# Performance work log

Hardware: AMD Instinct MI355X
Metric: run time of the kernel (lower is better)

## Reference

```python
import jax, jax.numpy as jnp
import numpy as np

B, C_IN, C_OUT, N, E = 4, 16, 16, 16384, 131072
EDGE_CH = 2 * (C_IN + 2)  # 36


def setup_inputs() -> dict:
    key = jax.random.key(0)
    ks = jax.random.split(key, 7)
    u = jax.random.normal(ks[0], (B, C_IN, N), dtype=jnp.float32)
    grid = jax.random.uniform(ks[1], (B, N, 2), dtype=jnp.float32)
    edge_index = jax.random.randint(ks[2], (2, E), 0, N, dtype=jnp.int32)
    k_w1 = jax.random.normal(ks[3], (EDGE_CH, 8), dtype=jnp.float32) / np.sqrt(EDGE_CH)
    k_b1 = jnp.zeros((8,), dtype=jnp.float32)
    k_w2 = jax.random.normal(ks[4], (8, C_IN * C_OUT), dtype=jnp.float32) / np.sqrt(8.0)
    k_b2 = jnp.zeros((C_IN * C_OUT,), dtype=jnp.float32)
    root_w = jax.random.normal(ks[5], (C_IN, C_OUT), dtype=jnp.float32) / np.sqrt(C_IN)
    return {"u": u, "grid": grid, "edge_index": edge_index,
            "k_w1": k_w1, "k_b1": k_b1, "k_w2": k_w2, "k_b2": k_b2,
            "root_w": root_w}


def reference(u, grid, edge_index, k_w1, k_b1, k_w2, k_b2, root_w):
    b, c_in, n = u.shape
    c_out = root_w.shape[1]
    # [B, C, N] -> [B*N, C]
    x = jnp.transpose(u, (0, 2, 1)).reshape(b * n, c_in)
    pf = jnp.concatenate([x, grid.reshape(-1, 2)], axis=-1)  # [B*N, C+2]
    # faithful to edge_index_one.repeat(1,1,B).view(2,-1): tile, NO batch offset
    ei = jnp.tile(edge_index, (1, b))  # [2, E*B]
    src, dst = ei[0], ei[1]
    attr = jnp.concatenate([pf[src], pf[dst]], axis=-1)  # [EB, 2*(C+2)]
    h = jax.nn.gelu(attr @ k_w1 + k_b1, approximate=False)
    w = (h @ k_w2 + k_b2).reshape(-1, c_in, c_out)  # [EB, C_in, C_out]
    msg = jnp.einsum('ec,eco->eo', x[src], w)  # per-edge matmul
    # scatter-mean onto targets (PyG aggr='mean'; empty -> 0)
    num_seg = b * n
    agg = jax.ops.segment_sum(msg, dst, num_segments=num_seg)
    cnt = jax.ops.segment_sum(jnp.ones((msg.shape[0],), msg.dtype), dst,
                              num_segments=num_seg)
    agg = agg / jnp.maximum(cnt, 1.0)[:, None]
    out = agg + x @ root_w  # root_weight=True, bias=False
    return jnp.transpose(out.reshape(b, n, c_out), (0, 2, 1))
```

## Files before the change

### kernel.cpp

```cpp
#include <hip/hip_runtime.h>
#include <math.h>

#define NN 16384
#define NE 131072
#define STRIDE 40

typedef unsigned int uint32;
typedef unsigned short ushort;

__device__ __forceinline__ ushort f2bf(float f) {
    uint32 b = __float_as_uint(f);
    b += 0x7FFFu + ((b >> 16) & 1u);
    return (ushort)(b >> 16);
}
__device__ __forceinline__ float bf2f(ushort u) {
    return __uint_as_float(((uint32)u) << 16);
}


__global__ __launch_bounds__(256) void d1_pre(
        const float* __restrict__ u, const float* __restrict__ grid,
        const float* __restrict__ kw1, const float* __restrict__ kb1,
        const float* __restrict__ kw2, const float* __restrict__ kb2,
        const float* __restrict__ root_w,
        float* __restrict__ H, float* __restrict__ Bterm,
        ushort* __restrict__ Gh, int* __restrict__ cursor,
        float* __restrict__ out) {
    int bid = blockIdx.x;
    int t = threadIdx.x;

    if (bid < 256) {
        __shared__ float s_pf[64 * 18];
        __shared__ float s_w1[288];
        __shared__ float s_b1[8];
        __shared__ float s_w2t[16 * 132];
        __shared__ float s_b2t[256];
        int n0 = bid * 64;

        if (t < 64) cursor[n0 + t] = 0;

        for (int i = t; i < 1024; i += 256) {
            int c = i >> 6, nl = i & 63;
            s_pf[nl * 18 + c] = u[c * NN + n0 + nl];
        }
        if (t < 128) {
            int nl = t >> 1, g = t & 1;
            s_pf[nl * 18 + 16 + g] = grid[2 * (n0 + nl) + g];
        }
        if (t < 8) s_b1[t] = kb1[t];
        {
            s_w1[t] = kw1[t];
            if (t < 32) s_w1[256 + t] = kw1[256 + t];
        }
        for (int i = t; i < 2048; i += 256) {
            int j = i >> 8, rem = i & 255, ci = rem >> 4, co = rem & 15;
            s_w2t[co * 132 + j * 16 + ci] = kw2[i];
        }
        {
            int ci = t >> 4, co = t & 15;
            s_b2t[co * 16 + ci] = kb2[ci * 16 + co];
        }
        __syncthreads();

        int co = t & 15;
        #pragma unroll
        for (int s = 0; s < 4; ++s) {
            int nl = s * 16 + (t >> 4);
            int n = n0 + nl;
            const float* pfl = s_pf + nl * 18;
            float x[16];
            #pragma unroll
            for (int ci = 0; ci < 16; ++ci) x[ci] = pfl[ci];

            {
                float bt = 0.0f;
                const float4* bv = (const float4*)(s_b2t + co * 16);
                #pragma unroll
                for (int q = 0; q < 4; ++q) {
                    float4 w = bv[q];
                    bt += x[4*q] * w.x + x[4*q+1] * w.y + x[4*q+2] * w.z + x[4*q+3] * w.w;
                }
                Bterm[n * 16 + co] = bt;
            }
            #pragma unroll
            for (int j = 0; j < 8; ++j) {
                float g = 0.0f;
                const float4* wv = (const float4*)(s_w2t + co * 132 + j * 16);
                #pragma unroll
                for (int q = 0; q < 4; ++q) {
                    float4 w = wv[q];
                    g += x[4*q] * w.x + x[4*q+1] * w.y + x[4*q+2] * w.z + x[4*q+3] * w.w;
                }
                Gh[(size_t)n * 128 + j * 16 + co] = f2bf(g);
            }
            if (co < 8) {
                float hv = s_b1[co];
                #pragma unroll
                for (int i = 0; i < 18; ++i) hv += pfl[i] * s_w1[i * 8 + co];
                H[n * 16 + co] = hv;
            } else {
                int jj = co - 8;
                float hv = 0.0f;
                #pragma unroll
                for (int i = 0; i < 18; ++i) hv += pfl[i] * s_w1[(18 + i) * 8 + jj];
                H[n * 16 + co] = hv;
            }
        }
    } else {
        __shared__ float s_rw[256];
        s_rw[t] = root_w[t];
        __syncthreads();
        int idx = (bid - 256) * 256 + t;
        int b = (idx >> 14) + 1;
        int n = idx & (NN - 1);
        float xx[16];
        #pragma unroll
        for (int c = 0; c < 16; ++c) xx[c] = u[(b * 16 + c) * NN + n];
        float acc[16];
        #pragma unroll
        for (int co = 0; co < 16; ++co) acc[co] = 0.0f;
        #pragma unroll
        for (int c = 0; c < 16; ++c) {
            float xv = xx[c];
            #pragma unroll
            for (int co = 0; co < 16; ++co) acc[co] += xv * s_rw[c * 16 + co];
        }
        #pragma unroll
        for (int co = 0; co < 16; ++co) out[(b * 16 + co) * NN + n] = acc[co];
    }
}

__global__ __launch_bounds__(256) void d2_edge(
        const int* __restrict__ ei,
        const float* __restrict__ H, const float* __restrict__ Bterm,
        const ushort* __restrict__ Gh,
        int* __restrict__ cursor, float* __restrict__ ebuf) {
    int e = blockIdx.x * 256 + threadIdx.x;
    int src = ei[e];
    int dst = ei[NE + e];

    const float4* hs = (const float4*)(H + src * 16);
    const float4* hd = (const float4*)(H + dst * 16 + 8);
    float4 a0 = hs[0], a1 = hs[1], b0 = hd[0], b1 = hd[1];
    float pre[8] = { a0.x + b0.x, a0.y + b0.y, a0.z + b0.z, a0.w + b0.w,
                     a1.x + b1.x, a1.y + b1.y, a1.z + b1.z, a1.w + b1.w };
    float h[8];
    #pragma unroll
    for (int j = 0; j < 8; ++j)
        h[j] = 0.5f * pre[j] * (1.0f + erff(pre[j] * 0.70710678118654752f));

    float msg[16];
    const float4* btv = (const float4*)(Bterm + src * 16);
    #pragma unroll
    for (int q = 0; q < 4; ++q) {
        float4 w = btv[q];
        msg[4*q] = w.x; msg[4*q+1] = w.y; msg[4*q+2] = w.z; msg[4*q+3] = w.w;
    }
    const uint32* gv = (const uint32*)(Gh + (size_t)src * 128);
    #pragma unroll
    for (int j = 0; j < 8; ++j) {
        float hj = h[j];
        #pragma unroll
        for (int q = 0; q < 8; ++q) {
            uint32 pk = gv[j * 8 + q];
            float g0 = __uint_as_float(pk << 16);
            float g1 = __uint_as_float(pk & 0xFFFF0000u);
            msg[2*q]   += hj * g0;
            msg[2*q+1] += hj * g1;
        }
    }
    int pos = atomicAdd(&cursor[dst], 1);
    if (pos < STRIDE) {
        float4* o = (float4*)(ebuf + ((size_t)dst * STRIDE + pos) * 16);
        #pragma unroll
        for (int q = 0; q < 4; ++q)
            o[q] = make_float4(msg[4*q], msg[4*q+1], msg[4*q+2], msg[4*q+3]);
    }
}

__global__ __launch_bounds__(256) void d3_out(
        const int* __restrict__ cursor, const float* __restrict__ ebuf,
        const float* __restrict__ u, const float* __restrict__ root_w,
        float* __restrict__ out) {
    __shared__ float s_rw[256];
    __shared__ float s_o[256];
    int t = threadIdx.x;
    s_rw[t] = root_w[t];
    __syncthreads();
    int n0 = blockIdx.x * 16;
    int nl = t >> 4, co = t & 15;
    int n = n0 + nl;
    int cnt = cursor[n];
    int deg = min(cnt, STRIDE);
    const float* base = ebuf + (size_t)n * STRIDE * 16 + co;
    float sum = 0.0f;
    for (int k = 0; k < deg; ++k) sum += base[k * 16];
    float acc = sum / fmaxf((float)cnt, 1.0f);
    #pragma unroll
    for (int c = 0; c < 16; ++c) acc += u[c * NN + n] * s_rw[c * 16 + co];
    s_o[co * 16 + nl] = acc;
    __syncthreads();
    int co2 = t >> 4, nl2 = t & 15;
    out[co2 * NN + n0 + nl2] = s_o[co2 * 16 + nl2];
}

extern "C" void kernel_launch(void* const* d_in, const int* in_sizes, int n_in,
                              void* d_out, int out_size, void* d_ws, size_t ws_size,
                              hipStream_t stream) {
    const float* u      = (const float*)d_in[0];
    const float* grid   = (const float*)d_in[1];
    const int*   ei     = (const int*)  d_in[2];
    const float* kw1    = (const float*)d_in[3];
    const float* kb1    = (const float*)d_in[4];
    const float* kw2    = (const float*)d_in[5];
    const float* kb2    = (const float*)d_in[6];
    const float* root_w = (const float*)d_in[7];
    float* out = (float*)d_out;

    float*  H      = (float*)d_ws;
    float*  Bterm  = H + NN * 16;
    ushort* Gh     = (ushort*)(Bterm + NN * 16);
    float*  ebuf   = (float*)(Gh + (size_t)NN * 128);
    int*    cursor = (int*)(ebuf + (size_t)NN * STRIDE * 16);

    d1_pre<<<256 + 192, 256, 0, stream>>>(u, grid, kw1, kb1, kw2, kb2, root_w,
                                          H, Bterm, Gh, cursor, out);
    d2_edge<<<512, 256, 0, stream>>>(ei, H, Bterm, Gh, cursor, ebuf);
    d3_out<<<NN / 16, 256, 0, stream>>>(cursor, ebuf, u, root_w, out);
}
```

Before: 42.77 us.

## Bucket edges by source and process each source's edges with a 16-lane group

Adds a scatter kernel that builds per-source destination lists, then restructures the edge kernel so 16 lanes share one source node's packed row (H, Bterm and G stored together in bf16), loading G once per source instead of once per edge. Each lane computes one output channel and one GELU hidden unit, with shuffles to broadcast. H and Bterm now go to bf16 as well, which trades some accuracy for smaller reads. The cost is an extra kernel launch with atomics, imbalance across sources with different degrees, and edges past 40 per source are dropped.

```diff
diff --git a/kernel.cpp b/kernel.cpp
--- a/kernel.cpp
+++ b/kernel.cpp
@@ -3,7 +3,7 @@
 
 #define NN 16384
 #define NE 131072
-#define STRIDE 40
+#define S2 40
 
 typedef unsigned int uint32;
 typedef unsigned short ushort;
@@ -12,9 +12,6 @@
     uint32 b = __float_as_uint(f);
     b += 0x7FFFu + ((b >> 16) & 1u);
     return (ushort)(b >> 16);
-}
-__device__ __forceinline__ float bf2f(ushort u) {
-    return __uint_as_float(((uint32)u) << 16);
 }
 
 
@@ -23,8 +20,7 @@
         const float* __restrict__ kw1, const float* __restrict__ kb1,
         const float* __restrict__ kw2, const float* __restrict__ kb2,
         const float* __restrict__ root_w,
-        float* __restrict__ H, float* __restrict__ Bterm,
-        ushort* __restrict__ Gh, int* __restrict__ cursor,
+        ushort* __restrict__ R, int* __restrict__ cursor, int* __restrict__ scur,
         float* __restrict__ out) {
     int bid = blockIdx.x;
     int t = threadIdx.x;
@@ -38,6 +34,7 @@
         int n0 = bid * 64;
 
         if (t < 64) cursor[n0 + t] = 0;
+        else if (t < 128) scur[n0 + t - 64] = 0;
 
         for (int i = t; i < 1024; i += 256) {
             int c = i >> 6, nl = i & 63;
@@ -67,6 +64,7 @@
         for (int s = 0; s < 4; ++s) {
             int nl = s * 16 + (t >> 4);
             int n = n0 + nl;
+            ushort* row = R + (size_t)n * 160;
             const float* pfl = s_pf + nl * 18;
             float x[16];
             #pragma unroll
@@ -80,30 +78,39 @@
                     float4 w = bv[q];
                     bt += x[4*q] * w.x + x[4*q+1] * w.y + x[4*q+2] * w.z + x[4*q+3] * w.w;
                 }
-                Bterm[n * 16 + co] = bt;
+                row[16 + co] = f2bf(bt);
             }
-            #pragma unroll
-            for (int j = 0; j < 8; ++j) {
-                float g = 0.0f;
-                const float4* wv = (const float4*)(s_w2t + co * 132 + j * 16);
-                #pragma unroll
-                for (int q = 0; q < 4; ++q) {
-                    float4 w = wv[q];
-                    g += x[4*q] * w.x + x[4*q+1] * w.y + x[4*q+2] * w.z + x[4*q+3] * w.w;
+            {
+                ushort gp[8];
+                #pragma unroll
+                for (int j = 0; j < 8; ++j) {
+                    float g = 0.0f;
+                    const float4* wv = (const float4*)(s_w2t + co * 132 + j * 16);
+                    #pragma unroll
+                    for (int q = 0; q < 4; ++q) {
+                        float4 w = wv[q];
+                        g += x[4*q] * w.x + x[4*q+1] * w.y + x[4*q+2] * w.z + x[4*q+3] * w.w;
+                    }
+                    gp[j] = f2bf(g);
                 }
-                Gh[(size_t)n * 128 + j * 16 + co] = f2bf(g);
+                uint4 pk;
+                pk.x = (uint32)gp[0] | ((uint32)gp[1] << 16);
+                pk.y = (uint32)gp[2] | ((uint32)gp[3] << 16);
+                pk.z = (uint32)gp[4] | ((uint32)gp[5] << 16);
+                pk.w = (uint32)gp[6] | ((uint32)gp[7] << 16);
+                *(uint4*)(row + 32 + co * 8) = pk;
             }
             if (co < 8) {
                 float hv = s_b1[co];
                 #pragma unroll
                 for (int i = 0; i < 18; ++i) hv += pfl[i] * s_w1[i * 8 + co];
-                H[n * 16 + co] = hv;
+                row[co] = f2bf(hv);
             } else {
                 int jj = co - 8;
                 float hv = 0.0f;
                 #pragma unroll
                 for (int i = 0; i < 18; ++i) hv += pfl[i] * s_w1[(18 + i) * 8 + jj];
-                H[n * 16 + co] = hv;
+                row[co] = f2bf(hv);
             }
         }
     } else {
@@ -130,51 +137,67 @@
     }
 }
 
+__global__ __launch_bounds__(256) void k_scatter(const int* __restrict__ ei,
+                                                 int* __restrict__ scur,
+                                                 int* __restrict__ sdst) {
+    int e = blockIdx.x * 256 + threadIdx.x;
+    int s = ei[e];
+    int d = ei[NE + e];
+    int pos = atomicAdd(&scur[s], 1);
+    if (pos < S2) sdst[s * S2 + pos] = d;
+}
+
 __global__ __launch_bounds__(256) void d2_edge(
-        const int* __restrict__ ei,
-        const float* __restrict__ H, const float* __restrict__ Bterm,
-        const ushort* __restrict__ Gh,
+        const ushort* __restrict__ R,
+        const int* __restrict__ sdst, const int* __restrict__ scur,
         int* __restrict__ cursor, float* __restrict__ ebuf) {
-    int e = blockIdx.x * 256 + threadIdx.x;
-    int src = ei[e];
-    int dst = ei[NE + e];
-
-    const float4* hs = (const float4*)(H + src * 16);
-    const float4* hd = (const float4*)(H + dst * 16 + 8);
-    float4 a0 = hs[0], a1 = hs[1], b0 = hd[0], b1 = hd[1];
-    float pre[8] = { a0.x + b0.x, a0.y + b0.y, a0.z + b0.z, a0.w + b0.w,
-                     a1.x + b1.x, a1.y + b1.y, a1.z + b1.z, a1.w + b1.w };
-    float h[8];
-    #pragma unroll
-    for (int j = 0; j < 8; ++j)
-        h[j] = 0.5f * pre[j] * (1.0f + erff(pre[j] * 0.70710678118654752f));
-
-    float msg[16];
-    const float4* btv = (const float4*)(Bterm + src * 16);
-    #pragma unroll
-    for (int q = 0; q < 4; ++q) {
-        float4 w = btv[q];
-        msg[4*q] = w.x; msg[4*q+1] = w.y; msg[4*q+2] = w.z; msg[4*q+3] = w.w;
-    }
-    const uint32* gv = (const uint32*)(Gh + (size_t)src * 128);
-    #pragma unroll
-    for (int j = 0; j < 8; ++j) {
-        float hj = h[j];
-        #pragma unroll
-        for (int q = 0; q < 8; ++q) {
-            uint32 pk = gv[j * 8 + q];
-            float g0 = __uint_as_float(pk << 16);
-            float g1 = __uint_as_float(pk & 0xFFFF0000u);
-            msg[2*q]   += hj * g0;
-            msg[2*q+1] += hj * g1;
-        }
-    }
-    int pos = atomicAdd(&cursor[dst], 1);
-    if (pos < STRIDE) {
-        float4* o = (float4*)(ebuf + ((size_t)dst * STRIDE + pos) * 16);
-        #pragma unroll
-        for (int q = 0; q < 4; ++q)
-            o[q] = make_float4(msg[4*q], msg[4*q+1], msg[4*q+2], msg[4*q+3]);
+    int t = threadIdx.x;
+    int k = t & 15;
+    int s = blockIdx.x * 16 + (t >> 4);
+
+    const ushort* row = R + (size_t)s * 160;
+    int j = k & 7;
+    float htj;
+    {
+        uint4 ht = *(const uint4*)(row);
+        uint32 uu = ((j >> 2) & 1) ? (((j >> 1) & 1) ? ht.w : ht.z)
+                                   : (((j >> 1) & 1) ? ht.y : ht.x);
+        htj = (j & 1) ? __uint_as_float(uu & 0xFFFF0000u) : __uint_as_float(uu << 16);
+    }
+    float btk = __uint_as_float(((uint32)row[16 + k]) << 16);
+    float Gk[8];
+    {
+        uint4 g = *(const uint4*)(row + 32 + k * 8);
+        Gk[0] = __uint_as_float(g.x << 16); Gk[1] = __uint_as_float(g.x & 0xFFFF0000u);
+        Gk[2] = __uint_as_float(g.y << 16); Gk[3] = __uint_as_float(g.y & 0xFFFF0000u);
+        Gk[4] = __uint_as_float(g.z << 16); Gk[5] = __uint_as_float(g.z & 0xFFFF0000u);
+        Gk[6] = __uint_as_float(g.w << 16); Gk[7] = __uint_as_float(g.w & 0xFFFF0000u);
+    }
+
+    int deg = min(scur[s], S2);
+    const int* sd = sdst + s * S2;
+    int my_sd = (k < deg) ? sd[k] : 0;
+
+    for (int i = 0; i < deg; ++i) {
+        int d = (i < 16) ? __shfl(my_sd, i, 16) : sd[i];
+        const ushort* rowd = R + (size_t)d * 160;
+        uint4 hb = *(const uint4*)(rowd + 8);
+        uint32 uu = ((j >> 2) & 1) ? (((j >> 1) & 1) ? hb.w : hb.z)
+                                   : (((j >> 1) & 1) ? hb.y : hb.x);
+        float hbj = (j & 1) ? __uint_as_float(uu & 0xFFFF0000u) : __uint_as_float(uu << 16);
+        float pre = htj + hbj;
+        float myh = 0.5f * pre * (1.0f + erff(pre * 0.70710678118654752f));
+
+        float msg = btk;
+        #pragma unroll
+        for (int jj = 0; jj < 8; ++jj)
+            msg += __shfl(myh, jj, 16) * Gk[jj];
+
+        int pos = 0;
+        if (k == 0) pos = atomicAdd(&cursor[d], 1);
+        pos = __shfl(pos, 0, 16);
+        if (pos < S2)
+            ebuf[((size_t)d * S2 + pos) * 16 + k] = msg;
     }
 }
 
@@ -191,8 +214,8 @@
     int nl = t >> 4, co = t & 15;
     int n = n0 + nl;
     int cnt = cursor[n];
-    int deg = min(cnt, STRIDE);
-    const float* base = ebuf + (size_t)n * STRIDE * 16 + co;
+    int deg = min(cnt, S2);
+    const float* base = ebuf + (size_t)n * S2 * 16 + co;
     float sum = 0.0f;
     for (int k = 0; k < deg; ++k) sum += base[k * 16];
     float acc = sum / fmaxf((float)cnt, 1.0f);
@@ -217,14 +240,15 @@
     const float* root_w = (const float*)d_in[7];
     float* out = (float*)d_out;
 
-    float*  H      = (float*)d_ws;
-    float*  Bterm  = H + NN * 16;
-    ushort* Gh     = (ushort*)(Bterm + NN * 16);
-    float*  ebuf   = (float*)(Gh + (size_t)NN * 128);
-    int*    cursor = (int*)(ebuf + (size_t)NN * STRIDE * 16);
+    ushort* R      = (ushort*)d_ws;
+    int*    sdst   = (int*)(R + (size_t)NN * 160);
+    float*  ebuf   = (float*)(sdst + (size_t)NN * S2);
+    int*    cursor = (int*)(ebuf + (size_t)NN * S2 * 16);
+    int*    scur   = cursor + NN;
 
     d1_pre<<<256 + 192, 256, 0, stream>>>(u, grid, kw1, kb1, kw2, kb2, root_w,
-                                          H, Bterm, Gh, cursor, out);
-    d2_edge<<<512, 256, 0, stream>>>(ei, H, Bterm, Gh, cursor, ebuf);
+                                          R, cursor, scur, out);
+    k_scatter<<<NE / 256, 256, 0, stream>>>(ei, scur, sdst);
+    d2_edge<<<NN / 16, 256, 0, stream>>>(R, sdst, scur, cursor, ebuf);
     d3_out<<<NN / 16, 256, 0, stream>>>(cursor, ebuf, u, root_w, out);
 }
```

New measurement: 59.28 us. 38.6% more time.

## Bucket edges by source node and pack per-node bf16 weights for locality

Applied to the files above, without the earlier changes.

Edges are first bucketed by source node with atomic cursors inside the precompute kernel, so the edge kernel processes all out-edges of a source together and neighbouring threads read the same per-node weight tables, improving cache reuse. The per-node bias term is stored as bf16 and packed with the G matrix into one contiguous 144-element record, transposed so each output channel's 8 values load as a single 16-byte vector. A separate zeroing kernel for both cursor arrays and an extra launch are added. Sources with more than 40 out-edges would have edges dropped, and the bias term now loses precision to bf16.

```diff
diff --git a/kernel.cpp b/kernel.cpp
--- a/kernel.cpp
+++ b/kernel.cpp
@@ -3,7 +3,7 @@
 
 #define NN 16384
 #define NE 131072
-#define STRIDE 40
+#define S2 40
 
 typedef unsigned int uint32;
 typedef unsigned short ushort;
@@ -13,18 +13,20 @@
     b += 0x7FFFu + ((b >> 16) & 1u);
     return (ushort)(b >> 16);
 }
-__device__ __forceinline__ float bf2f(ushort u) {
-    return __uint_as_float(((uint32)u) << 16);
-}
-
-
-__global__ __launch_bounds__(256) void d1_pre(
+
+
+__global__ __launch_bounds__(256) void k0_zero(int4* __restrict__ p) {
+    p[blockIdx.x * 256 + threadIdx.x] = make_int4(0, 0, 0, 0);
+}
+
+__global__ __launch_bounds__(256) void k1_pre(
         const float* __restrict__ u, const float* __restrict__ grid,
+        const int* __restrict__ ei,
         const float* __restrict__ kw1, const float* __restrict__ kb1,
         const float* __restrict__ kw2, const float* __restrict__ kb2,
         const float* __restrict__ root_w,
-        float* __restrict__ H, float* __restrict__ Bterm,
-        ushort* __restrict__ Gh, int* __restrict__ cursor,
+        float* __restrict__ H, ushort* __restrict__ GB,
+        int* __restrict__ scur, int* __restrict__ sdst,
         float* __restrict__ out) {
     int bid = blockIdx.x;
     int t = threadIdx.x;
@@ -37,8 +39,6 @@
         __shared__ float s_b2t[256];
         int n0 = bid * 64;
 
-        if (t < 64) cursor[n0 + t] = 0;
-
         for (int i = t; i < 1024; i += 256) {
             int c = i >> 6, nl = i & 63;
             s_pf[nl * 18 + c] = u[c * NN + n0 + nl];
@@ -67,6 +67,7 @@
         for (int s = 0; s < 4; ++s) {
             int nl = s * 16 + (t >> 4);
             int n = n0 + nl;
+            ushort* gb = GB + (size_t)n * 144;
             const float* pfl = s_pf + nl * 18;
             float x[16];
             #pragma unroll
@@ -80,18 +81,27 @@
                     float4 w = bv[q];
                     bt += x[4*q] * w.x + x[4*q+1] * w.y + x[4*q+2] * w.z + x[4*q+3] * w.w;
                 }
-                Bterm[n * 16 + co] = bt;
+                gb[co] = f2bf(bt);
             }
-            #pragma unroll
-            for (int j = 0; j < 8; ++j) {
-                float g = 0.0f;
-                const float4* wv = (const float4*)(s_w2t + co * 132 + j * 16);
-                #pragma unroll
-                for (int q = 0; q < 4; ++q) {
-                    float4 w = wv[q];
-                    g += x[4*q] * w.x + x[4*q+1] * w.y + x[4*q+2] * w.z + x[4*q+3] * w.w;
+            {
+                ushort gp[8];
+                #pragma unroll
+                for (int j = 0; j < 8; ++j) {
+                    float g = 0.0f;
+                    const float4* wv = (const float4*)(s_w2t + co * 132 + j * 16);
+                    #pragma unroll
+                    for (int q = 0; q < 4; ++q) {
+                        float4 w = wv[q];
+                        g += x[4*q] * w.x + x[4*q+1] * w.y + x[4*q+2] * w.z + x[4*q+3] * w.w;
+                    }
+                    gp[j] = f2bf(g);
                 }
-                Gh[(size_t)n * 128 + j * 16 + co] = f2bf(g);
+                uint4 pk;
+                pk.x = (uint32)gp[0] | ((uint32)gp[1] << 16);
+                pk.y = (uint32)gp[2] | ((uint32)gp[3] << 16);
+                pk.z = (uint32)gp[4] | ((uint32)gp[5] << 16);
+                pk.w = (uint32)gp[6] | ((uint32)gp[7] << 16);
+                *(uint4*)(gb + 16 + co * 8) = pk;
             }
             if (co < 8) {
                 float hv = s_b1[co];
@@ -106,7 +116,7 @@
                 H[n * 16 + co] = hv;
             }
         }
-    } else {
+    } else if (bid < 448) {
         __shared__ float s_rw[256];
         s_rw[t] = root_w[t];
         __syncthreads();
@@ -127,20 +137,32 @@
         }
         #pragma unroll
         for (int co = 0; co < 16; ++co) out[(b * 16 + co) * NN + n] = acc[co];
-    }
-}
-
-__global__ __launch_bounds__(256) void d2_edge(
-        const int* __restrict__ ei,
-        const float* __restrict__ H, const float* __restrict__ Bterm,
-        const ushort* __restrict__ Gh,
+    } else {
+        int e = (bid - 448) * 256 + t;
+        int s = ei[e];
+        int d = ei[NE + e];
+        int pos = atomicAdd(&scur[s], 1);
+        if (pos < S2) sdst[s * S2 + pos] = d;
+    }
+}
+
+__global__ __launch_bounds__(320) void k2_edge(
+        const float* __restrict__ H, const ushort* __restrict__ GB,
+        const int* __restrict__ sdst, const int* __restrict__ scur,
         int* __restrict__ cursor, float* __restrict__ ebuf) {
-    int e = blockIdx.x * 256 + threadIdx.x;
-    int src = ei[e];
-    int dst = ei[NE + e];
-
-    const float4* hs = (const float4*)(H + src * 16);
-    const float4* hd = (const float4*)(H + dst * 16 + 8);
+    int t = threadIdx.x;
+    int sl = t / S2;
+    int slot = t - sl * S2;
+    int s = blockIdx.x * 8 + sl;
+
+    int deg = scur[s];
+    if (deg > S2) deg = S2;
+    if (slot >= deg) return;
+
+    int d = sdst[s * S2 + slot];
+
+    const float4* hs = (const float4*)(H + s * 16);
+    const float4* hd = (const float4*)(H + d * 16 + 8);
     float4 a0 = hs[0], a1 = hs[1], b0 = hd[0], b1 = hd[1];
     float pre[8] = { a0.x + b0.x, a0.y + b0.y, a0.z + b0.z, a0.w + b0.w,
                      a1.x + b1.x, a1.y + b1.y, a1.z + b1.z, a1.w + b1.w };
@@ -149,36 +171,46 @@
     for (int j = 0; j < 8; ++j)
         h[j] = 0.5f * pre[j] * (1.0f + erff(pre[j] * 0.70710678118654752f));
 
+    const ushort* gb = GB + (size_t)s * 144;
     float msg[16];
-    const float4* btv = (const float4*)(Bterm + src * 16);
+    {
+        uint4 bt0 = *(const uint4*)(gb);
+        uint4 bt1 = *(const uint4*)(gb + 8);
+        msg[0]  = __uint_as_float(bt0.x << 16); msg[1]  = __uint_as_float(bt0.x & 0xFFFF0000u);
+        msg[2]  = __uint_as_float(bt0.y << 16); msg[3]  = __uint_as_float(bt0.y & 0xFFFF0000u);
+        msg[4]  = __uint_as_float(bt0.z << 16); msg[5]  = __uint_as_float(bt0.z & 0xFFFF0000u);
+        msg[6]  = __uint_as_float(bt0.w << 16); msg[7]  = __uint_as_float(bt0.w & 0xFFFF0000u);
+        msg[8]  = __uint_as_float(bt1.x << 16); msg[9]  = __uint_as_float(bt1.x & 0xFFFF0000u);
+        msg[10] = __uint_as_float(bt1.y << 16); msg[11] = __uint_as_float(bt1.y & 0xFFFF0000u);
+        msg[12] = __uint_as_float(bt1.z << 16); msg[13] = __uint_as_float(bt1.z & 0xFFFF0000u);
+        msg[14] = __uint_as_float(bt1.w << 16); msg[15] = __uint_as_float(bt1.w & 0xFFFF0000u);
+    }
     #pragma unroll
-    for (int q = 0; q < 4; ++q) {
-        float4 w = btv[q];
-        msg[4*q] = w.x; msg[4*q+1] = w.y; msg[4*q+2] = w.z; msg[4*q+3] = w.w;
-    }
-    const uint32* gv = (const uint32*)(Gh + (size_t)src * 128);
-    #pragma unroll
-    for (int j = 0; j < 8; ++j) {
-        float hj = h[j];
-        #pragma unroll
-        for (int q = 0; q < 8; ++q) {
-            uint32 pk = gv[j * 8 + q];
-            float g0 = __uint_as_float(pk << 16);
-            float g1 = __uint_as_float(pk & 0xFFFF0000u);
-            msg[2*q]   += hj * g0;
-            msg[2*q+1] += hj * g1;
-        }
-    }
-    int pos = atomicAdd(&cursor[dst], 1);
-    if (pos < STRIDE) {
-        float4* o = (float4*)(ebuf + ((size_t)dst * STRIDE + pos) * 16);
-        #pragma unroll
-        for (int q = 0; q < 4; ++q)
-            o[q] = make_float4(msg[4*q], msg[4*q+1], msg[4*q+2], msg[4*q+3]);
-    }
-}
-
-__global__ __launch_bounds__(256) void d3_out(
+    for (int co = 0; co < 16; ++co) {
+        uint4 g = *(const uint4*)(gb + 16 + co * 8);
+        float acc = msg[co];
+        acc += h[0] * __uint_as_float(g.x << 16);
+        acc += h[1] * __uint_as_float(g.x & 0xFFFF0000u);
+        acc += h[2] * __uint_as_float(g.y << 16);
+        acc += h[3] * __uint_as_float(g.y & 0xFFFF0000u);
+        acc += h[4] * __uint_as_float(g.z << 16);
+        acc += h[5] * __uint_as_float(g.z & 0xFFFF0000u);
+        acc += h[6] * __uint_as_float(g.w << 16);
+        acc += h[7] * __uint_as_float(g.w & 0xFFFF0000u);
+        msg[co] = acc;
+    }
+
+    int pos = atomicAdd(&cursor[d], 1);
+    if (pos < S2) {
+        float4* o = (float4*)(ebuf + ((size_t)d * S2 + pos) * 16);
+        o[0] = make_float4(msg[0],  msg[1],  msg[2],  msg[3]);
+        o[1] = make_float4(msg[4],  msg[5],  msg[6],  msg[7]);
+        o[2] = make_float4(msg[8],  msg[9],  msg[10], msg[11]);
+        o[3] = make_float4(msg[12], msg[13], msg[14], msg[15]);
+    }
+}
+
+__global__ __launch_bounds__(256) void k3_out(
         const int* __restrict__ cursor, const float* __restrict__ ebuf,
         const float* __restrict__ u, const float* __restrict__ root_w,
         float* __restrict__ out) {
@@ -191,8 +223,8 @@
     int nl = t >> 4, co = t & 15;
     int n = n0 + nl;
     int cnt = cursor[n];
-    int deg = min(cnt, STRIDE);
-    const float* base = ebuf + (size_t)n * STRIDE * 16 + co;
+    int deg = min(cnt, S2);
+    const float* base = ebuf + (size_t)n * S2 * 16 + co;
     float sum = 0.0f;
     for (int k = 0; k < deg; ++k) sum += base[k * 16];
     float acc = sum / fmaxf((float)cnt, 1.0f);
@@ -218,13 +250,16 @@
     float* out = (float*)d_out;
 
     float*  H      = (float*)d_ws;
-    float*  Bterm  = H + NN * 16;
-    ushort* Gh     = (ushort*)(Bterm + NN * 16);
-    float*  ebuf   = (float*)(Gh + (size_t)NN * 128);
-    int*    cursor = (int*)(ebuf + (size_t)NN * STRIDE * 16);
-
-    d1_pre<<<256 + 192, 256, 0, stream>>>(u, grid, kw1, kb1, kw2, kb2, root_w,
-                                          H, Bterm, Gh, cursor, out);
-    d2_edge<<<512, 256, 0, stream>>>(ei, H, Bterm, Gh, cursor, ebuf);
-    d3_out<<<NN / 16, 256, 0, stream>>>(cursor, ebuf, u, root_w, out);
-}
+    ushort* GB     = (ushort*)(H + NN * 16);
+    int*    sdst   = (int*)(GB + (size_t)NN * 144);
+    float*  ebuf   = (float*)(sdst + (size_t)NN * S2);
+    int*    cursor = (int*)(ebuf + (size_t)NN * S2 * 16);
+
+    int* scur = cursor + NN;
+
+    k0_zero<<<32, 256, 0, stream>>>((int4*)cursor);
+    k1_pre<<<960, 256, 0, stream>>>(u, grid, ei, kw1, kb1, kw2, kb2, root_w,
+                                    H, GB, scur, sdst, out);
+    k2_edge<<<NN / 8, 320, 0, stream>>>(H, GB, sdst, scur, cursor, ebuf);
+    k3_out<<<NN / 16, 256, 0, stream>>>(cursor, ebuf, u, root_w, out);
+}
```

After: 59.63 us. +39.4%, slower.
